# Performance work log

Hardware: AMD Instinct MI355X
Metric: run time of the kernel (lower is better)

Reference implementation:

```python
import jax, jax.numpy as jnp
import numpy as np

HIDDEN = 64

def setup_inputs() -> dict:
    key = jax.random.key(0)
    ks = jax.random.split(key, 7)
    B, T, D, C = 2048, 1024, 32, 10
    s_ih = 1.0 / np.sqrt(HIDDEN)
    return {
        "x": jax.random.normal(ks[0], (B, T, D), dtype=jnp.float32),
        "W_ih": jax.random.normal(ks[1], (4 * HIDDEN, D), dtype=jnp.float32) * s_ih,
        "W_hh": jax.random.normal(ks[2], (4 * HIDDEN, HIDDEN), dtype=jnp.float32) * s_ih,
        "b_ih": jax.random.normal(ks[3], (4 * HIDDEN,), dtype=jnp.float32) * s_ih,
        "b_hh": jax.random.normal(ks[4], (4 * HIDDEN,), dtype=jnp.float32) * s_ih,
        "fc_W": jax.random.normal(ks[5], (C, HIDDEN), dtype=jnp.float32) * s_ih,
        "fc_b": jax.random.normal(ks[6], (C,), dtype=jnp.float32) * s_ih,
    }

def _lstm_last_hidden(x, W_ih, W_hh, b_ih, b_hh):
    B = x.shape[0]
    H = HIDDEN
    # Precompute input projections for all timesteps: [T, B, 4H]
    xg = jnp.einsum('btd,gd->tbg', x, W_ih) + (b_ih + b_hh)

    def step(carry, xg_t):
        h, c = carry
        gates = xg_t + h @ W_hh.T  # [B, 4H]
        i = jax.nn.sigmoid(gates[:, 0 * H:1 * H])
        f = jax.nn.sigmoid(gates[:, 1 * H:2 * H])
        g = jnp.tanh(gates[:, 2 * H:3 * H])
        o = jax.nn.sigmoid(gates[:, 3 * H:4 * H])
        c = f * c + i * g
        h = o * jnp.tanh(c)
        return (h, c), None

    h0 = jnp.zeros((B, H), dtype=x.dtype)
    c0 = jnp.zeros((B, H), dtype=x.dtype)
    (h_last, _), _ = jax.lax.scan(step, (h0, c0), xg)
    return h_last

def reference(x, W_ih, W_hh, b_ih, b_hh, fc_W, fc_b):
    last_hidden = _lstm_last_hidden(x, W_ih, W_hh, b_ih, b_hh)  # [B, H]
    logits = last_hidden @ fc_W.T + fc_b  # [B, C]
    return logits
```

## Files before the change

kernel.cpp:

```cpp
#include <hip/hip_runtime.h>
#include <hip/hip_bf16.h>
#include <stdint.h>

#define DD 32
#define HH 64
#define HSTRIDE 80
#define LOG2E 1.44269504088896340736f

typedef float f32x4 __attribute__((ext_vector_type(4)));
typedef short s16x8 __attribute__((ext_vector_type(8)));

__device__ __forceinline__ uint32_t cvtpk(float lo, float hi) {
  uint32_t r;
  asm("v_cvt_pk_bf16_f32 %0, %1, %2" : "=v"(r) : "v"(lo), "v"(hi));
  return r;
}

#define BAR() do {                                                    \
  asm volatile("s_waitcnt lgkmcnt(0)\n\ts_barrier" ::: "memory");     \
  __builtin_amdgcn_sched_barrier(0);                                  \
} while (0)

__global__ __launch_bounds__(256, 2)
void lstm_fused(const float* __restrict__ x,
                const float* __restrict__ W_ih,
                const float* __restrict__ W_hh,
                const float* __restrict__ b_ih,
                const float* __restrict__ b_hh,
                const float* __restrict__ fc_W,
                const float* __restrict__ fc_b,
                float* __restrict__ out,
                int T)
{
  const int tid   = threadIdx.x;
  const int w     = tid >> 6;
  const int lane  = tid & 63;
  const int lr    = lane & 15;
  const int lq    = lane >> 4;
  const int arow  = lr >> 2;
  const int bm    = blockIdx.x * 4;

  __shared__ __align__(16) uint16_t hbuf[2][4 * HSTRIDE];

  s16x8 Bx[4], Bh0[4], Bh1[4];
  f32x4 biasv[4];
  #pragma unroll
  for (int j = 0; j < 4; ++j) {
    const int n = 64 * j + 16 * w + lr;
    const float sc = (j == 2) ? (2.0f * LOG2E) : LOG2E;
    {
      const float* p = W_ih + n * DD + lq * 8;
      f32x4 a = *(const f32x4*)p;
      f32x4 b = *(const f32x4*)(p + 4);
      union { uint32_t u[4]; s16x8 s; } pk;
      pk.u[0] = cvtpk(a[0]*sc, a[1]*sc); pk.u[1] = cvtpk(a[2]*sc, a[3]*sc);
      pk.u[2] = cvtpk(b[0]*sc, b[1]*sc); pk.u[3] = cvtpk(b[2]*sc, b[3]*sc);
      Bx[j] = pk.s;
    }
    {
      const float* p = W_hh + n * HH + lq * 8;
      f32x4 a = *(const f32x4*)p;
      f32x4 b = *(const f32x4*)(p + 4);
      union { uint32_t u[4]; s16x8 s; } pk;
      pk.u[0] = cvtpk(a[0]*sc, a[1]*sc); pk.u[1] = cvtpk(a[2]*sc, a[3]*sc);
      pk.u[2] = cvtpk(b[0]*sc, b[1]*sc); pk.u[3] = cvtpk(b[2]*sc, b[3]*sc);
      Bh0[j] = pk.s;
    }
    {
      const float* p = W_hh + n * HH + 32 + lq * 8;
      f32x4 a = *(const f32x4*)p;
      f32x4 b = *(const f32x4*)(p + 4);
      union { uint32_t u[4]; s16x8 s; } pk;
      pk.u[0] = cvtpk(a[0]*sc, a[1]*sc); pk.u[1] = cvtpk(a[2]*sc, a[3]*sc);
      pk.u[2] = cvtpk(b[0]*sc, b[1]*sc); pk.u[3] = cvtpk(b[2]*sc, b[3]*sc);
      Bh1[j] = pk.s;
    }
    const float bb = (b_ih[n] + b_hh[n]) * sc;
    biasv[j] = (f32x4){bb, bb, bb, bb};
  }

  for (int i = tid; i < 2 * 4 * HSTRIDE; i += 256) ((uint16_t*)hbuf)[i] = 0;

  float c = 0.f;

  const int roff0 = arow * HSTRIDE + 8 * lq;
  const int roff1 = roff0 + 32;
  const int woff  = lq * HSTRIDE + 16 * w + lr;

  const float* xbase = x + (size_t)(bm + arow) * (size_t)T * DD + lq * 8;
  f32x4 xa0 = *(const f32x4*)xbase;        f32x4 xb0 = *(const f32x4*)(xbase + 4);
  f32x4 xa1 = *(const f32x4*)(xbase + DD); f32x4 xb1 = *(const f32x4*)(xbase + DD + 4);
  const float* xp = xbase + 2 * DD;

  __syncthreads();

  auto step = [&](f32x4& xa, f32x4& xb, bool pf,
                  const uint16_t* hr, uint16_t* hw) {
    BAR();

    s16x8 ah0 = *(const s16x8*)(hr + roff0);
    s16x8 ah1 = *(const s16x8*)(hr + roff1);

    union { uint32_t u[4]; s16x8 s; } ax;
    ax.u[0] = cvtpk(xa[0], xa[1]); ax.u[1] = cvtpk(xa[2], xa[3]);
    ax.u[2] = cvtpk(xb[0], xb[1]); ax.u[3] = cvtpk(xb[2], xb[3]);
    if (pf) {
      xa = *(const f32x4*)xp; xb = *(const f32x4*)(xp + 4); xp += DD;
    }

    f32x4 acc[4];
    #pragma unroll
    for (int j = 0; j < 4; ++j)
      acc[j] = __builtin_amdgcn_mfma_f32_16x16x32_bf16(ax.s, Bx[j], biasv[j], 0, 0, 0);
    #pragma unroll
    for (int j = 0; j < 4; ++j)
      acc[j] = __builtin_amdgcn_mfma_f32_16x16x32_bf16(ah0, Bh0[j], acc[j], 0, 0, 0);
    #pragma unroll
    for (int j = 0; j < 4; ++j)
      acc[j] = __builtin_amdgcn_mfma_f32_16x16x32_bf16(ah1, Bh1[j], acc[j], 0, 0, 0);

    float g0 = acc[0][0], g1 = acc[1][0], g2 = acc[2][0], g3 = acc[3][0];

    float A = __builtin_amdgcn_exp2f(-g0);
    float F = __builtin_amdgcn_exp2f(-g1);
    float Q = __builtin_amdgcn_exp2f(g2);
    float O = __builtin_amdgcn_exp2f(-g3);
    float u  = 1.f + A;
    float v  = 1.f + Q;
    float wf = 1.f + F;
    float M  = u * v;
    float D  = M * wf;
    float num = c * M + (Q - 1.f) * wf;
    float r  = __builtin_amdgcn_rcpf(D);
    c = num * r;
    float sarg = fminf(fmaxf((2.0f * LOG2E) * c, -80.f), 80.f);
    float S  = __builtin_amdgcn_exp2f(sarg);
    float r2 = __builtin_amdgcn_rcpf((1.f + O) * (1.f + S));
    float hv = (S - 1.f) * r2;
    hw[woff] = (uint16_t)cvtpk(hv, hv);
  };

  for (int t = 0; t < T - 2; t += 2) {
    step(xa0, xb0, true, hbuf[0], hbuf[1]);
    step(xa1, xb1, true, hbuf[1], hbuf[0]);
  }
  step(xa0, xb0, false, hbuf[0], hbuf[1]);
  step(xa1, xb1, false, hbuf[1], hbuf[0]);

  __syncthreads();

  if (tid < 40) {
    const int m = tid / 10, cl = tid % 10;
    float s = fc_b[cl];
    const float* wr = fc_W + cl * HH;
    const uint16_t* hm = hbuf[0] + m * HSTRIDE;
    #pragma unroll
    for (int k = 0; k < HH; ++k) {
      union { uint32_t u; float f; } v;
      v.u = (uint32_t)hm[k] << 16;
      s += v.f * wr[k];
    }
    out[(size_t)(bm + m) * 10 + cl] = s;
  }
}

extern "C" void kernel_launch(void* const* d_in, const int* in_sizes, int n_in,
                              void* d_out, int out_size, void* d_ws, size_t ws_size,
                              hipStream_t stream) {
  const float* x    = (const float*)d_in[0];
  const float* W_ih = (const float*)d_in[1];
  const float* W_hh = (const float*)d_in[2];
  const float* b_ih = (const float*)d_in[3];
  const float* b_hh = (const float*)d_in[4];
  const float* fc_W = (const float*)d_in[5];
  const float* fc_b = (const float*)d_in[6];
  float* out = (float*)d_out;

  const int B = out_size / 10;
  const int T = in_sizes[0] / (B * DD);

  dim3 grid(B / 4), block(256);
  hipLaunchKernelGGL(lstm_fused, grid, block, 0, stream,
                     x, W_ih, W_hh, b_ih, b_hh, fc_W, fc_b, out, T);
}
```

Baseline: 346.4 us.

## Software-pipeline input projection MFMAs one step ahead of recurrent chain

```diff
diff --git a/kernel.cpp b/kernel.cpp
--- a/kernel.cpp
+++ b/kernel.cpp
@@ -87,11 +87,24 @@
   const int roff1 = roff0 + 32;
   const int woff  = lq * HSTRIDE + 16 * w + lr;
 
+  const f32x4 zz = {0.f, 0.f, 0.f, 0.f};
+
   const float* xbase = x + (size_t)(bm + arow) * (size_t)T * DD + lq * 8;
   f32x4 xa0 = *(const f32x4*)xbase;        f32x4 xb0 = *(const f32x4*)(xbase + 4);
   f32x4 xa1 = *(const f32x4*)(xbase + DD); f32x4 xb1 = *(const f32x4*)(xbase + DD + 4);
   const float* xp = xbase + 2 * DD;
 
+  f32x4 accx[4];
+  {
+    union { uint32_t u[4]; s16x8 s; } ax;
+    ax.u[0] = cvtpk(xa0[0], xa0[1]); ax.u[1] = cvtpk(xa0[2], xa0[3]);
+    ax.u[2] = cvtpk(xb0[0], xb0[1]); ax.u[3] = cvtpk(xb0[2], xb0[3]);
+    #pragma unroll
+    for (int j = 0; j < 4; ++j)
+      accx[j] = __builtin_amdgcn_mfma_f32_16x16x32_bf16(ax.s, Bx[j], biasv[j], 0, 0, 0);
+    xa0 = *(const f32x4*)xp; xb0 = *(const f32x4*)(xp + 4); xp += DD;
+  }
+
   __syncthreads();
 
   auto step = [&](f32x4& xa, f32x4& xb, bool pf,
@@ -100,26 +113,18 @@
 
     s16x8 ah0 = *(const s16x8*)(hr + roff0);
     s16x8 ah1 = *(const s16x8*)(hr + roff1);
-
-    union { uint32_t u[4]; s16x8 s; } ax;
-    ax.u[0] = cvtpk(xa[0], xa[1]); ax.u[1] = cvtpk(xa[2], xa[3]);
-    ax.u[2] = cvtpk(xb[0], xb[1]); ax.u[3] = cvtpk(xb[2], xb[3]);
-    if (pf) {
-      xa = *(const f32x4*)xp; xb = *(const f32x4*)(xp + 4); xp += DD;
-    }
-
-    f32x4 acc[4];
-    #pragma unroll
-    for (int j = 0; j < 4; ++j)
-      acc[j] = __builtin_amdgcn_mfma_f32_16x16x32_bf16(ax.s, Bx[j], biasv[j], 0, 0, 0);
-    #pragma unroll
-    for (int j = 0; j < 4; ++j)
-      acc[j] = __builtin_amdgcn_mfma_f32_16x16x32_bf16(ah0, Bh0[j], acc[j], 0, 0, 0);
-    #pragma unroll
-    for (int j = 0; j < 4; ++j)
-      acc[j] = __builtin_amdgcn_mfma_f32_16x16x32_bf16(ah1, Bh1[j], acc[j], 0, 0, 0);
-
-    float g0 = acc[0][0], g1 = acc[1][0], g2 = acc[2][0], g3 = acc[3][0];
+    f32x4 acch[4];
+    #pragma unroll
+    for (int j = 0; j < 4; ++j)
+      acch[j] = __builtin_amdgcn_mfma_f32_16x16x32_bf16(ah0, Bh0[j], zz, 0, 0, 0);
+    #pragma unroll
+    for (int j = 0; j < 4; ++j)
+      acch[j] = __builtin_amdgcn_mfma_f32_16x16x32_bf16(ah1, Bh1[j], acch[j], 0, 0, 0);
+
+    float g0 = accx[0][0] + acch[0][0];
+    float g1 = accx[1][0] + acch[1][0];
+    float g2 = accx[2][0] + acch[2][0];
+    float g3 = accx[3][0] + acch[3][0];
 
     float A = __builtin_amdgcn_exp2f(-g0);
     float F = __builtin_amdgcn_exp2f(-g1);
@@ -130,22 +135,34 @@
     float wf = 1.f + F;
     float M  = u * v;
     float D  = M * wf;
-    float num = c * M + (Q - 1.f) * wf;
+    float num = fmaf(c, M, (Q - 1.f) * wf);
     float r  = __builtin_amdgcn_rcpf(D);
     c = num * r;
-    float sarg = fminf(fmaxf((2.0f * LOG2E) * c, -80.f), 80.f);
+    float sarg = __builtin_amdgcn_fmed3f((2.0f * LOG2E) * c, -80.f, 80.f);
     float S  = __builtin_amdgcn_exp2f(sarg);
     float r2 = __builtin_amdgcn_rcpf((1.f + O) * (1.f + S));
     float hv = (S - 1.f) * r2;
     hw[woff] = (uint16_t)cvtpk(hv, hv);
+
+    union { uint32_t u[4]; s16x8 s; } ax;
+    ax.u[0] = cvtpk(xa[0], xa[1]); ax.u[1] = cvtpk(xa[2], xa[3]);
+    ax.u[2] = cvtpk(xb[0], xb[1]); ax.u[3] = cvtpk(xb[2], xb[3]);
+    if (pf) {
+      xa = *(const f32x4*)xp; xb = *(const f32x4*)(xp + 4); xp += DD;
+    }
+    #pragma unroll
+    for (int j = 0; j < 4; ++j)
+      accx[j] = __builtin_amdgcn_mfma_f32_16x16x32_bf16(ax.s, Bx[j], biasv[j], 0, 0, 0);
   };
 
-  for (int t = 0; t < T - 2; t += 2) {
-    step(xa0, xb0, true, hbuf[0], hbuf[1]);
-    step(xa1, xb1, true, hbuf[1], hbuf[0]);
-  }
-  step(xa0, xb0, false, hbuf[0], hbuf[1]);
-  step(xa1, xb1, false, hbuf[1], hbuf[0]);
+  for (int t = 0; t < T - 4; t += 2) {
+    step(xa1, xb1, true, hbuf[0], hbuf[1]);
+    step(xa0, xb0, true, hbuf[1], hbuf[0]);
+  }
+  step(xa1, xb1, true,  hbuf[0], hbuf[1]);
+  step(xa0, xb0, false, hbuf[1], hbuf[0]);
+  step(xa1, xb1, false, hbuf[0], hbuf[1]);
+  step(xa0, xb0, false, hbuf[1], hbuf[0]);
 
   __syncthreads();
 
```

New measurement: 375.0 us. +8.3%, slower.
